# Kernel optimization log

Measured on AMD Instinct MI355X. Metric: run time of the kernel, lower is better.

The kernel has to match this reference:

```python
import jax, jax.numpy as jnp
import numpy as np

B, N, D, R = 2, 256, 128, 32

def _sh_l1(r):
    # e3nn-style component-normalized l=1 spherical harmonics of unit vectors
    return jnp.sqrt(3.0) * r

def _sh_l2(r):
    x, y, z = r[..., 0], r[..., 1], r[..., 2]
    c = jnp.sqrt(15.0)
    return jnp.stack([
        c * x * y,
        c * y * z,
        0.5 * jnp.sqrt(5.0) * (3.0 * z * z - 1.0),  # x^2+y^2+z^2 = 1
        c * x * z,
        0.5 * c * (x * x - y * y),
    ], axis=-1)

def _radial(rbf, w1, b1, w2, b2):
    h = rbf @ w1 + b1
    return (h * jax.nn.sigmoid(h)) @ w2 + b2  # Linear -> SiLU -> Linear

def _layernorm(x, g, b, eps=1e-5):
    m = jnp.mean(x, axis=-1, keepdims=True)
    v = jnp.var(x, axis=-1, keepdims=True)
    return (x - m) * jax.lax.rsqrt(v + eps) * g + b

def setup_inputs() -> dict:
    key = jax.random.key(0)
    ks = iter(jax.random.split(key, 40))
    def nrm(shape, s=1.0):
        return jax.random.normal(next(ks), shape, dtype=jnp.float32) * s
    r_hat = nrm((B, N, N, 3))
    r_hat = r_hat / (jnp.linalg.norm(r_hat, axis=-1, keepdims=True) + 1e-9)
    inp = {
        'node_s': nrm((B, N, D)),
        'node_v': nrm((B, N, 3, D)),
        'node_t': nrm((B, N, 5, D)),
        'rbf': jax.random.uniform(next(ks), (B, N, N, R), dtype=jnp.float32),
        'r_hat': r_hat,
        'mask': jnp.ones((B, N, N), dtype=jnp.float32),
    }
    s1, s2 = 1.0 / np.sqrt(R), 1.0 / np.sqrt(D)
    for p in ('r0', 'r1', 'r2', 'r110'):
        inp[p + '_w1'] = nrm((R, D), s1)
        inp[p + '_b1'] = jnp.zeros((D,), jnp.float32)
        inp[p + '_w2'] = nrm((D, D), s2)
        inp[p + '_b2'] = jnp.zeros((D,), jnp.float32)
    inp['src_w'] = nrm((D, D), s2)
    inp['ln_g'] = jnp.ones((D,), jnp.float32)
    inp['ln_b'] = jnp.zeros((D,), jnp.float32)
    inp['out_w'] = nrm((D, D), s2)
    inp['out_b'] = jnp.zeros((D,), jnp.float32)
    inp['v_scale'] = jnp.ones((D,), jnp.float32)
    inp['t_scale'] = jnp.ones((D,), jnp.float32)
    return inp

def reference(node_s, node_v, node_t, rbf, r_hat, mask,
              r0_w1, r0_b1, r0_w2, r0_b2,
              r1_w1, r1_b1, r1_w2, r1_b2,
              r2_w1, r2_b1, r2_w2, r2_b2,
              r110_w1, r110_b1, r110_w2, r110_b2,
              src_w, ln_g, ln_b, out_w, out_b, v_scale, t_scale):
    h = node_s @ src_w                               # (B,N,D)
    h_j = h[:, None, :, :] * mask[..., None]         # (B,N,N,D): h_j[b,i,j]=h[b,j]*mask[b,i,j]
    Y1 = _sh_l1(r_hat)                               # (B,N,N,3)
    Y2 = _sh_l2(r_hat)                               # (B,N,N,5)

    msg_s = jnp.sum(h_j * _radial(rbf, r0_w1, r0_b1, r0_w2, r0_b2), axis=2)  # (B,N,D)
    delta_v = jnp.einsum('bijd,bijc->bicd',
                         h_j * _radial(rbf, r1_w1, r1_b1, r1_w2, r1_b2), Y1) * v_scale
    delta_t = jnp.einsum('bijd,bijc->bicd',
                         h_j * _radial(rbf, r2_w1, r2_b1, r2_w2, r2_b2), Y2) * t_scale

    # v_j[b,i,j] = node_v[b,i] (per the torch unsqueeze(2).expand)
    dot_vY1 = jnp.einsum('bicd,bijc->bijd', node_v, Y1)                      # (B,N,N,D)
    msg_s_from_v = jnp.sum(dot_vY1 * _radial(rbf, r110_w1, r110_b1, r110_w2, r110_b2)
                           * mask[..., None], axis=2)                        # (B,N,D)

    delta_s = _layernorm(msg_s + msg_s_from_v, ln_g, ln_b) @ out_w + out_b
    return (delta_s, delta_v, delta_t)
```

## Files before the change

kernel.cpp:

```cpp
#include <hip/hip_runtime.h>

#define Bb 2
#define Nn 256
#define Dd 128
#define Rr 32

typedef unsigned short u16;
typedef unsigned int   u32;
typedef __attribute__((ext_vector_type(8))) short bf16x8;
typedef __attribute__((ext_vector_type(4))) short bf16x4;
typedef __attribute__((ext_vector_type(4))) float f32x4;
typedef __attribute__((ext_vector_type(2))) u32   u32x2;
typedef __attribute__((ext_vector_type(4))) u32   u32x4;

__device__ u16 g_w1t[4*Dd*Rr];
__device__ u16 g_w2t[4*Dd*Dd];

__device__ __forceinline__ short f2bfs(float f){
  u32 u = __float_as_uint(f);
  u += 0x7FFFu + ((u >> 16) & 1u);
  return (short)(u >> 16);
}
__device__ __forceinline__ u16 f2bf(float f){
  u32 u = __float_as_uint(f);
  u += 0x7FFFu + ((u >> 16) & 1u);
  return (u16)(u >> 16);
}
__device__ __forceinline__ u32 cvtpk(float a, float b){
  u32 r;
  asm("v_cvt_pk_bf16_f32 %0, %1, %2" : "=v"(r) : "v"(a), "v"(b));
  return r;
}
__device__ __forceinline__ int swz(int j){
  return (j&3) | ((((j>>2)^(j>>3))&1)<<2);
}

__global__ __launch_bounds__(128) void prep_kernel(
    const float* __restrict__ node_s, const float* __restrict__ src_w,
    const float* __restrict__ r0w1, const float* __restrict__ r1w1,
    const float* __restrict__ r2w1, const float* __restrict__ r3w1,
    const float* __restrict__ r0w2, const float* __restrict__ r1w2,
    const float* __restrict__ r2w2, const float* __restrict__ r3w2,
    float* __restrict__ h_out)
{
  const int bx = blockIdx.x;
  const int t  = threadIdx.x;
  if (bx < Bb*Nn){
    __shared__ float s_row[Dd];
    s_row[t] = node_s[(size_t)bx*Dd + t];
    __syncthreads();
    float acc = 0.f;
    #pragma unroll 8
    for (int k=0;k<Dd;k++) acc += s_row[k]*src_w[k*Dd + t];
    h_out[(size_t)bx*Dd + t] = acc;
  } else {
    const int kb = bx - Bb*Nn;
    const int p  = kb >> 3, sl = kb & 7;
    const float* W1 = (p==0)?r0w1:(p==1)?r1w1:(p==2)?r2w1:r3w1;
    const float* W2 = (p==0)?r0w2:(p==1)?r1w2:(p==2)?r2w2:r3w2;
    u16* W1T = g_w1t + p*Dd*Rr;
    u16* W2T = g_w2t + p*Dd*Dd;
    #pragma unroll
    for (int it=0; it<4; it++){
      int in = sl*512 + it*128 + t;
      W1T[(in & 127)*Rr + (in >> 7)] = f2bf(W1[in]);
    }
    #pragma unroll
    for (int it=0; it<16; it++){
      int in = sl*2048 + it*128 + t;
      W2T[(in & 127)*Dd + (in >> 7)] = f2bf(W2[in]);
    }
  }
}

__global__ __launch_bounds__(512,4) void se3_mfma12(
    const float* __restrict__ node_v,
    const float* __restrict__ rbf,
    const float* __restrict__ r_hat,
    const float* __restrict__ maskp,
    const float* __restrict__ r0b1, const float* __restrict__ r0b2,
    const float* __restrict__ r1b1, const float* __restrict__ r1b2,
    const float* __restrict__ r2b1, const float* __restrict__ r2b2,
    const float* __restrict__ r3b1, const float* __restrict__ r3b2,
    const float* __restrict__ ln_g, const float* __restrict__ ln_b,
    const float* __restrict__ out_w, const float* __restrict__ out_b,
    const float* __restrict__ v_scale, const float* __restrict__ t_scale,
    const float* __restrict__ h_ws,
    float* __restrict__ out_s, float* __restrict__ out_v, float* __restrict__ out_t)
{
  __shared__ u16   s_rbf[Nn*36];
  __shared__ u16   s_hid[2*64*128];
  __shared__ u16   s_YT[10*264];
  __shared__ u16   s_Y1r[3*264];
  __shared__ float s_msg[Dd];
  __shared__ float s_xn[Dd];
  __shared__ float s_part[4*Dd];
  __shared__ float s_mv[2];

  const int tid  = threadIdx.x;
  const int bi   = blockIdx.x;
  const int b    = bi >> 8;
  const int lane = tid & 63;
  const int w    = tid >> 6;
  const int q    = lane >> 4;
  const int cc   = lane & 15;
  const int dwb  = w*16;

  if (tid < Nn){
    int j = tid;
    size_t pidx = (size_t)bi*Nn + j;
    float mk = maskp[pidx];
    float x = r_hat[pidx*3+0];
    float y = r_hat[pidx*3+1];
    float z = r_hat[pidx*3+2];
    const float SQ3=1.7320508075688772f;
    const float C15=3.8729833462074170f;
    const float C5H=1.1180339887498949f;
    float y1a=SQ3*x, y1b=SQ3*y, y1c=SQ3*z;
    s_YT[0*264+j]=f2bf(mk);
    s_YT[1*264+j]=f2bf(y1a*mk);
    s_YT[2*264+j]=f2bf(y1b*mk);
    s_YT[3*264+j]=f2bf(y1c*mk);
    s_YT[4*264+j]=f2bf(C15*x*y*mk);
    s_YT[5*264+j]=f2bf(C15*y*z*mk);
    s_YT[6*264+j]=f2bf(C5H*(3.f*z*z-1.f)*mk);
    s_YT[7*264+j]=f2bf(C15*x*z*mk);
    s_YT[8*264+j]=f2bf(0.5f*C15*(x*x-y*y)*mk);
    s_YT[9*264+j]=f2bf(mk);
    s_Y1r[0*264+j]=f2bf(y1a);
    s_Y1r[1*264+j]=f2bf(y1b);
    s_Y1r[2*264+j]=f2bf(y1c);
  }

  const float* rbf_blk = rbf + (size_t)bi*Nn*Rr;
  const float* hb      = h_ws + (size_t)b*Nn*Dd;

  for (int idx=tid; idx<Nn*Rr/2; idx+=512){
    int j = idx >> 4, r2 = (idx & 15)*2;
    const float* src = &rbf_blk[j*Rr + r2];
    float v0 = src[0], v1 = src[1];
    *(u32*)&s_rbf[j*36 + r2] = cvtpk(v0, v1);
  }

  bf16x8 vBf;
  {
    const float* nv = node_v + (size_t)bi*3*Dd;
    int dd = dwb+cc;
    bf16x8 t = {0,0,0,0,0,0,0,0};
    if (q==0){
      t[0]=f2bfs(nv[0*Dd+dd]);
      t[1]=f2bfs(nv[1*Dd+dd]);
      t[2]=f2bfs(nv[2*Dd+dd]);
    }
    vBf=t;
  }

  __syncthreads();

  const f32x4 zf = {0.f,0.f,0.f,0.f};
  f32x4 accred = zf;
  int buf = 0;

  #pragma unroll 1
  for (int p=0;p<4;p++){
    const float* B1p = (p==0)?r0b1:(p==1)?r1b1:(p==2)?r2b1:r3b1;
    const float* B2p = (p==0)?r0b2:(p==1)?r1b2:(p==2)?r2b2:r3b2;
    const u16* W1T = g_w1t + p*Dd*Rr;
    const u16* W2T = g_w2t + p*Dd*Dd;
    const int lo = (p==0)?0:(p==1)?1:(p==2)?4:9;
    const int hi = (p==0)?0:(p==1)?3:(p==2)?8:9;
    const u32 gmask = (cc>=lo && cc<=hi) ? 0xFFFFFFFFu : 0u;
    const u16* ytrow = &s_YT[(cc<10?cc:9)*264];

    bf16x8 w1f  = *(const bf16x8*)&W1T[(dwb+cc)*Rr + q*8];
    bf16x8 w2f[4];
    #pragma unroll
    for (int ks=0;ks<4;ks++)
      w2f[ks] = *(const bf16x8*)&W2T[(dwb+cc)*Dd + ks*32 + q*8];
    f32x4 b1v4 = *(const f32x4*)&B1p[dwb + q*4];
    float b2v  = B2p[dwb + cc];

    #pragma unroll 1
    for (int ch=0; ch<4; ch++){
      #pragma unroll 1
      for (int jt=0;jt<4;jt++){
        const int jrow = jt*16 + cc;
        const u16* bp = &s_rbf[(ch*64 + jrow)*36 + q*8];
        bf16x4 lo4 = *(const bf16x4*)bp;
        bf16x4 hi4 = *(const bf16x4*)(bp+4);
        bf16x8 rbff = {lo4[0],lo4[1],lo4[2],lo4[3],hi4[0],hi4[1],hi4[2],hi4[3]};
        f32x4 hc = __builtin_amdgcn_mfma_f32_16x16x32_bf16(w1f, rbff, zf, 0,0,0);
        float s[4];
        #pragma unroll
        for (int r=0;r<4;r++){
          float x  = hc[r] + b1v4[r];
          float e  = __expf(-x);
          s[r]     = x*__builtin_amdgcn_rcpf(1.f+e);
        }
        u32x2 pk = { cvtpk(s[0], s[1]), cvtpk(s[2], s[3]) };
        const int c0 = w*2 + (q>>1);
        *(u32x2*)&s_hid[buf*8192 + jrow*128 + ((c0 ^ swz(jrow))<<3) + (q&1)*4] = pk;
      }
      __syncthreads();

      #pragma unroll 1
      for (int g=0; g<2; g++){
        u32 bB[4];
        #pragma unroll 1
        for (int mm=0;mm<2;mm++){
          const int jp = g*32 + ((cc>>2)<<3) + mm*4 + (cc&3);
          bf16x8 af[4];
          #pragma unroll
          for (int ks=0;ks<4;ks++)
            af[ks] = *(const bf16x8*)&s_hid[buf*8192 + jp*128 + (((ks*4+q) ^ swz(jp))<<3)];

          f32x4 dotC;
          if (p==3){
            bf16x8 aY = {0,0,0,0,0,0,0,0};
            if (q==0){
              int jg = ch*64 + jp;
              aY[0]=(short)s_Y1r[0*264+jg];
              aY[1]=(short)s_Y1r[1*264+jg];
              aY[2]=(short)s_Y1r[2*264+jg];
            }
            dotC = __builtin_amdgcn_mfma_f32_16x16x32_bf16(aY, vBf, zf, 0,0,0);
          }

          f32x4 c2 = zf;
          #pragma unroll
          for (int ks=0;ks<4;ks++)
            c2 = __builtin_amdgcn_mfma_f32_16x16x32_bf16(af[ks], w2f[ks], c2, 0,0,0);
          const int dd = dwb+cc;
          float gg[4];
          if (p<3){
            const float* hp = hb + (size_t)(ch*64 + g*32 + q*8 + mm*4)*Dd + dd;
            #pragma unroll
            for (int r=0;r<4;r++)
              gg[r] = (c2[r]+b2v) * hp[(size_t)r*Dd];
          } else {
            #pragma unroll
            for (int r=0;r<4;r++)
              gg[r] = (c2[r]+b2v) * dotC[r];
          }
          bB[mm*2+0] = cvtpk(gg[0], gg[1]);
          bB[mm*2+1] = cvtpk(gg[2], gg[3]);
        }
        bf16x8 aR = *(const bf16x8*)(ytrow + ch*64 + g*32 + q*8);
        u32* arp = (u32*)&aR;
        arp[0]&=gmask; arp[1]&=gmask; arp[2]&=gmask; arp[3]&=gmask;
        u32x4 bw = { bB[0], bB[1], bB[2], bB[3] };
        bf16x8 bG = __builtin_bit_cast(bf16x8, bw);
        accred = __builtin_amdgcn_mfma_f32_16x16x32_bf16(aR, bG, accred, 0,0,0);
      }
      buf ^= 1;
    }
  }

  {
    const int d = dwb + cc;
    #pragma unroll
    for (int r=0;r<4;r++){
      const int rw = q*4 + r;
      float val = accred[r];
      if (rw==0)      s_msg[d] = val;
      else if (rw<=3) out_v[(size_t)bi*3*Dd + (size_t)(rw-1)*Dd + d] = val*v_scale[d];
      else if (rw<=8) out_t[(size_t)bi*5*Dd + (size_t)(rw-4)*Dd + d] = val*t_scale[d];
      else if (rw==9) s_xn[d] = val;
    }
  }
  __syncthreads();

  if (tid < 64){
    float a0=s_msg[tid]+s_xn[tid], a1=s_msg[tid+64]+s_xn[tid+64];
    float s1=a0+a1, s2=a0*a0+a1*a1;
    #pragma unroll
    for (int off=1;off<64;off<<=1){
      s1 += __shfl_xor(s1,off);
      s2 += __shfl_xor(s2,off);
    }
    if (tid==0){
      float m   = s1*(1.f/Dd);
      float var = fmaxf(s2*(1.f/Dd) - m*m, 0.f);
      s_mv[0]=m;
      s_mv[1]=rsqrtf(var+1e-5f);
    }
  }
  __syncthreads();
  if (tid < Dd){
    float msg = s_msg[tid]+s_xn[tid];
    s_xn[tid] = (msg - s_mv[0])*s_mv[1]*ln_g[tid] + ln_b[tid];
  }
  __syncthreads();

  {
    int dp = tid & 127, seg = tid >> 7;
    float pa = 0.f;
    #pragma unroll 8
    for (int k=seg*32;k<seg*32+32;k++)
      pa += s_xn[k]*out_w[k*Dd+dp];
    s_part[seg*Dd+dp]=pa;
  }
  __syncthreads();
  if (tid < Dd)
    out_s[(size_t)bi*Dd+tid] = s_part[tid]+s_part[Dd+tid]+s_part[2*Dd+tid]+s_part[3*Dd+tid]+out_b[tid];
}

extern "C" void kernel_launch(void* const* d_in, const int* in_sizes, int n_in,
                              void* d_out, int out_size, void* d_ws, size_t ws_size,
                              hipStream_t stream) {
  const float* node_s = (const float*)d_in[0];
  const float* node_v = (const float*)d_in[1];
  const float* rbf    = (const float*)d_in[3];
  const float* r_hat  = (const float*)d_in[4];
  const float* maskp  = (const float*)d_in[5];
  const float* r0w1=(const float*)d_in[6],  *r0b1=(const float*)d_in[7];
  const float* r0w2=(const float*)d_in[8],  *r0b2=(const float*)d_in[9];
  const float* r1w1=(const float*)d_in[10], *r1b1=(const float*)d_in[11];
  const float* r1w2=(const float*)d_in[12], *r1b2=(const float*)d_in[13];
  const float* r2w1=(const float*)d_in[14], *r2b1=(const float*)d_in[15];
  const float* r2w2=(const float*)d_in[16], *r2b2=(const float*)d_in[17];
  const float* r3w1=(const float*)d_in[18], *r3b1=(const float*)d_in[19];
  const float* r3w2=(const float*)d_in[20], *r3b2=(const float*)d_in[21];
  const float* src_w  =(const float*)d_in[22];
  const float* ln_g   =(const float*)d_in[23];
  const float* ln_b   =(const float*)d_in[24];
  const float* out_w  =(const float*)d_in[25];
  const float* out_b  =(const float*)d_in[26];
  const float* v_scale=(const float*)d_in[27];
  const float* t_scale=(const float*)d_in[28];

  float* h_ws = (float*)d_ws;
  float* out_s = (float*)d_out;
  float* out_v = out_s + (size_t)Bb*Nn*Dd;
  float* out_t = out_v + (size_t)Bb*Nn*3*Dd;

  prep_kernel<<<dim3(Bb*Nn + 32), dim3(128), 0, stream>>>(
      node_s, src_w,
      r0w1, r1w1, r2w1, r3w1, r0w2, r1w2, r2w2, r3w2,
      h_ws);
  se3_mfma12<<<dim3(Bb*Nn), dim3(512), 0, stream>>>(
      node_v, rbf, r_hat, maskp,
      r0b1,r0b2, r1b1,r1b2, r2b1,r2b2, r3b1,r3b2,
      ln_g, ln_b, out_w, out_b, v_scale, t_scale,
      h_ws, out_s, out_v, out_t);
}
```

Measured before the change: 187.9 us.

## Software-pipeline radial GEMM1 into next buffer and transpose h for vector loads

Flattens the radial-network and chunk loops into a single 16-step loop. Each step computes the next chunk's first GEMM and SiLU into the alternate hidden buffer while the current chunk's second GEMM and reduction run, leaving one barrier per step. The h workspace is now stored transposed (d-major), so each lane fetches its four h values with a single f32x4 load instead of four strided scalar loads. The rbf shared-memory row pitch goes from 36 to 40 so one 16-byte load replaces two 8-byte loads. The costs are higher register pressure from keeping both pipeline stages live and possible new LDS bank conflicts with the 40-element pitch.

```diff
diff --git a/kernel.cpp b/kernel.cpp
--- a/kernel.cpp
+++ b/kernel.cpp
@@ -8,7 +8,6 @@
 typedef unsigned short u16;
 typedef unsigned int   u32;
 typedef __attribute__((ext_vector_type(8))) short bf16x8;
-typedef __attribute__((ext_vector_type(4))) short bf16x4;
 typedef __attribute__((ext_vector_type(4))) float f32x4;
 typedef __attribute__((ext_vector_type(2))) u32   u32x2;
 typedef __attribute__((ext_vector_type(4))) u32   u32x4;
@@ -52,7 +51,8 @@
     float acc = 0.f;
     #pragma unroll 8
     for (int k=0;k<Dd;k++) acc += s_row[k]*src_w[k*Dd + t];
-    h_out[(size_t)bx*Dd + t] = acc;
+    const int b = bx >> 8, i = bx & 255;
+    h_out[(size_t)(b*Dd + t)*Nn + i] = acc;
   } else {
     const int kb = bx - Bb*Nn;
     const int p  = kb >> 3, sl = kb & 7;
@@ -73,7 +73,7 @@
   }
 }
 
-__global__ __launch_bounds__(512,4) void se3_mfma12(
+__global__ __launch_bounds__(512,4) void se3_mfma13(
     const float* __restrict__ node_v,
     const float* __restrict__ rbf,
     const float* __restrict__ r_hat,
@@ -88,7 +88,7 @@
     const float* __restrict__ h_ws,
     float* __restrict__ out_s, float* __restrict__ out_v, float* __restrict__ out_t)
 {
-  __shared__ u16   s_rbf[Nn*36];
+  __shared__ u16   s_rbf[Nn*40];
   __shared__ u16   s_hid[2*64*128];
   __shared__ u16   s_YT[10*264];
   __shared__ u16   s_Y1r[3*264];
@@ -133,13 +133,13 @@
   }
 
   const float* rbf_blk = rbf + (size_t)bi*Nn*Rr;
-  const float* hb      = h_ws + (size_t)b*Nn*Dd;
+  const float* htb     = h_ws + (size_t)b*Dd*Nn;
 
   for (int idx=tid; idx<Nn*Rr/2; idx+=512){
     int j = idx >> 4, r2 = (idx & 15)*2;
     const float* src = &rbf_blk[j*Rr + r2];
     float v0 = src[0], v1 = src[1];
-    *(u32*)&s_rbf[j*36 + r2] = cvtpk(v0, v1);
+    *(u32*)&s_rbf[j*40 + r2] = cvtpk(v0, v1);
   }
 
   bf16x8 vBf;
@@ -159,101 +159,110 @@
 
   const f32x4 zf = {0.f,0.f,0.f,0.f};
   f32x4 accred = zf;
+  const u16* ytrow = &s_YT[(cc<10?cc:9)*264];
+
+  auto do_gemm1 = [&](int chn, int bufn, const bf16x8& w1f_, const f32x4& b1v_){
+    #pragma unroll 1
+    for (int jt=0;jt<4;jt++){
+      const int jrow = jt*16 + cc;
+      bf16x8 rbff = *(const bf16x8*)&s_rbf[(chn*64 + jrow)*40 + q*8];
+      f32x4 hc = __builtin_amdgcn_mfma_f32_16x16x32_bf16(w1f_, rbff, zf, 0,0,0);
+      float s[4];
+      #pragma unroll
+      for (int r=0;r<4;r++){
+        float x  = hc[r] + b1v_[r];
+        float e  = __expf(-x);
+        s[r]     = x*__builtin_amdgcn_rcpf(1.f+e);
+      }
+      u32x2 pk = { cvtpk(s[0], s[1]), cvtpk(s[2], s[3]) };
+      const int c0 = w*2 + (q>>1);
+      *(u32x2*)&s_hid[bufn*8192 + jrow*128 + ((c0 ^ swz(jrow))<<3) + (q&1)*4] = pk;
+    }
+  };
+
   int buf = 0;
+  bf16x8 w1f;  f32x4 b1v4;
+  bf16x8 w2f[4]; float b2v; u32 gmask;
+
+  w1f  = *(const bf16x8*)&g_w1t[(dwb+cc)*Rr + q*8];
+  b1v4 = *(const f32x4*)&r0b1[dwb + q*4];
+  do_gemm1(0, 0, w1f, b1v4);
 
   #pragma unroll 1
-  for (int p=0;p<4;p++){
-    const float* B1p = (p==0)?r0b1:(p==1)?r1b1:(p==2)?r2b1:r3b1;
-    const float* B2p = (p==0)?r0b2:(p==1)?r1b2:(p==2)?r2b2:r3b2;
-    const u16* W1T = g_w1t + p*Dd*Rr;
-    const u16* W2T = g_w2t + p*Dd*Dd;
-    const int lo = (p==0)?0:(p==1)?1:(p==2)?4:9;
-    const int hi = (p==0)?0:(p==1)?3:(p==2)?8:9;
-    const u32 gmask = (cc>=lo && cc<=hi) ? 0xFFFFFFFFu : 0u;
-    const u16* ytrow = &s_YT[(cc<10?cc:9)*264];
-
-    bf16x8 w1f  = *(const bf16x8*)&W1T[(dwb+cc)*Rr + q*8];
-    bf16x8 w2f[4];
-    #pragma unroll
-    for (int ks=0;ks<4;ks++)
-      w2f[ks] = *(const bf16x8*)&W2T[(dwb+cc)*Dd + ks*32 + q*8];
-    f32x4 b1v4 = *(const f32x4*)&B1p[dwb + q*4];
-    float b2v  = B2p[dwb + cc];
+  for (int t=0;t<16;t++){
+    const int p = t>>2, ch = t&3;
+    if (ch==0){
+      const u16* W2T = g_w2t + p*Dd*Dd;
+      #pragma unroll
+      for (int ks=0;ks<4;ks++)
+        w2f[ks] = *(const bf16x8*)&W2T[(dwb+cc)*Dd + ks*32 + q*8];
+      const float* B2p = (p==0)?r0b2:(p==1)?r1b2:(p==2)?r2b2:r3b2;
+      b2v = B2p[dwb + cc];
+      const int lo = (p==0)?0:(p==1)?1:(p==2)?4:9;
+      const int hi = (p==0)?0:(p==1)?3:(p==2)?8:9;
+      gmask = (cc>=lo && cc<=hi) ? 0xFFFFFFFFu : 0u;
+    }
+    __syncthreads();
+
+    if (t<15){
+      const int tn=t+1, pn=tn>>2, chn=tn&3;
+      if (chn==0){
+        w1f  = *(const bf16x8*)&g_w1t[pn*Dd*Rr + (dwb+cc)*Rr + q*8];
+        const float* B1p = (pn==1)?r1b1:(pn==2)?r2b1:r3b1;
+        b1v4 = *(const f32x4*)&B1p[dwb + q*4];
+      }
+      do_gemm1(chn, buf^1, w1f, b1v4);
+    }
 
     #pragma unroll 1
-    for (int ch=0; ch<4; ch++){
+    for (int g=0; g<2; g++){
+      u32 bB[4];
       #pragma unroll 1
-      for (int jt=0;jt<4;jt++){
-        const int jrow = jt*16 + cc;
-        const u16* bp = &s_rbf[(ch*64 + jrow)*36 + q*8];
-        bf16x4 lo4 = *(const bf16x4*)bp;
-        bf16x4 hi4 = *(const bf16x4*)(bp+4);
-        bf16x8 rbff = {lo4[0],lo4[1],lo4[2],lo4[3],hi4[0],hi4[1],hi4[2],hi4[3]};
-        f32x4 hc = __builtin_amdgcn_mfma_f32_16x16x32_bf16(w1f, rbff, zf, 0,0,0);
-        float s[4];
+      for (int mm=0;mm<2;mm++){
+        const int jp = g*32 + ((cc>>2)<<3) + mm*4 + (cc&3);
+        bf16x8 af[4];
         #pragma unroll
-        for (int r=0;r<4;r++){
-          float x  = hc[r] + b1v4[r];
-          float e  = __expf(-x);
-          s[r]     = x*__builtin_amdgcn_rcpf(1.f+e);
+        for (int ks=0;ks<4;ks++)
+          af[ks] = *(const bf16x8*)&s_hid[buf*8192 + jp*128 + (((ks*4+q) ^ swz(jp))<<3)];
+
+        f32x4 dotC;
+        if (p==3){
+          bf16x8 aY = {0,0,0,0,0,0,0,0};
+          if (q==0){
+            int jg = ch*64 + jp;
+            aY[0]=(short)s_Y1r[0*264+jg];
+            aY[1]=(short)s_Y1r[1*264+jg];
+            aY[2]=(short)s_Y1r[2*264+jg];
+          }
+          dotC = __builtin_amdgcn_mfma_f32_16x16x32_bf16(aY, vBf, zf, 0,0,0);
         }
-        u32x2 pk = { cvtpk(s[0], s[1]), cvtpk(s[2], s[3]) };
-        const int c0 = w*2 + (q>>1);
-        *(u32x2*)&s_hid[buf*8192 + jrow*128 + ((c0 ^ swz(jrow))<<3) + (q&1)*4] = pk;
+
+        f32x4 c2 = zf;
+        #pragma unroll
+        for (int ks=0;ks<4;ks++)
+          c2 = __builtin_amdgcn_mfma_f32_16x16x32_bf16(af[ks], w2f[ks], c2, 0,0,0);
+        float gg[4];
+        if (p<3){
+          f32x4 hq = *(const f32x4*)&htb[(size_t)(dwb+cc)*Nn + ch*64 + g*32 + q*8 + mm*4];
+          #pragma unroll
+          for (int r=0;r<4;r++)
+            gg[r] = (c2[r]+b2v) * hq[r];
+        } else {
+          #pragma unroll
+          for (int r=0;r<4;r++)
+            gg[r] = (c2[r]+b2v) * dotC[r];
+        }
+        bB[mm*2+0] = cvtpk(gg[0], gg[1]);
+        bB[mm*2+1] = cvtpk(gg[2], gg[3]);
       }
-      __syncthreads();
-
-      #pragma unroll 1
-      for (int g=0; g<2; g++){
-        u32 bB[4];
-        #pragma unroll 1
-        for (int mm=0;mm<2;mm++){
-          const int jp = g*32 + ((cc>>2)<<3) + mm*4 + (cc&3);
-          bf16x8 af[4];
-          #pragma unroll
-          for (int ks=0;ks<4;ks++)
-            af[ks] = *(const bf16x8*)&s_hid[buf*8192 + jp*128 + (((ks*4+q) ^ swz(jp))<<3)];
-
-          f32x4 dotC;
-          if (p==3){
-            bf16x8 aY = {0,0,0,0,0,0,0,0};
-            if (q==0){
-              int jg = ch*64 + jp;
-              aY[0]=(short)s_Y1r[0*264+jg];
-              aY[1]=(short)s_Y1r[1*264+jg];
-              aY[2]=(short)s_Y1r[2*264+jg];
-            }
-            dotC = __builtin_amdgcn_mfma_f32_16x16x32_bf16(aY, vBf, zf, 0,0,0);
-          }
-
-          f32x4 c2 = zf;
-          #pragma unroll
-          for (int ks=0;ks<4;ks++)
-            c2 = __builtin_amdgcn_mfma_f32_16x16x32_bf16(af[ks], w2f[ks], c2, 0,0,0);
-          const int dd = dwb+cc;
-          float gg[4];
-          if (p<3){
-            const float* hp = hb + (size_t)(ch*64 + g*32 + q*8 + mm*4)*Dd + dd;
-            #pragma unroll
-            for (int r=0;r<4;r++)
-              gg[r] = (c2[r]+b2v) * hp[(size_t)r*Dd];
-          } else {
-            #pragma unroll
-            for (int r=0;r<4;r++)
-              gg[r] = (c2[r]+b2v) * dotC[r];
-          }
-          bB[mm*2+0] = cvtpk(gg[0], gg[1]);
-          bB[mm*2+1] = cvtpk(gg[2], gg[3]);
-        }
-        bf16x8 aR = *(const bf16x8*)(ytrow + ch*64 + g*32 + q*8);
-        u32* arp = (u32*)&aR;
-        arp[0]&=gmask; arp[1]&=gmask; arp[2]&=gmask; arp[3]&=gmask;
-        u32x4 bw = { bB[0], bB[1], bB[2], bB[3] };
-        bf16x8 bG = __builtin_bit_cast(bf16x8, bw);
-        accred = __builtin_amdgcn_mfma_f32_16x16x32_bf16(aR, bG, accred, 0,0,0);
-      }
-      buf ^= 1;
-    }
+      bf16x8 aR = *(const bf16x8*)(ytrow + ch*64 + g*32 + q*8);
+      u32* arp = (u32*)&aR;
+      arp[0]&=gmask; arp[1]&=gmask; arp[2]&=gmask; arp[3]&=gmask;
+      u32x4 bw = { bB[0], bB[1], bB[2], bB[3] };
+      bf16x8 bG = __builtin_bit_cast(bf16x8, bw);
+      accred = __builtin_amdgcn_mfma_f32_16x16x32_bf16(aR, bG, accred, 0,0,0);
+    }
+    buf ^= 1;
   }
 
   {
@@ -338,7 +347,7 @@
       node_s, src_w,
       r0w1, r1w1, r2w1, r3w1, r0w2, r1w2, r2w2, r3w2,
       h_ws);
-  se3_mfma12<<<dim3(Bb*Nn), dim3(512), 0, stream>>>(
+  se3_mfma13<<<dim3(Bb*Nn), dim3(512), 0, stream>>>(
       node_v, rbf, r_hat, maskp,
       r0b1,r0b2, r1b1,r1b2, r2b1,r2b2, r3b1,r3b2,
       ln_g, ln_b, out_w, out_b, v_scale, t_scale,
```

Result: no change. 184.5 us (-1.8%).
